# Kernel tuning notes

Measured on AMD Instinct MI355X. Metric: run time of the kernel, lower is better.

Reference implementation:

```python
import jax, jax.numpy as jnp
import numpy as np

EPS = 1e-5

def adain_norm(x):
    # per-(batch,channel) instance normalization over spatial dims (AdaIN projection)
    mean = jnp.mean(x, axis=(2, 3), keepdims=True)
    var = jnp.var(x, axis=(2, 3), keepdims=True)
    return (x - mean) / jnp.sqrt(var + EPS)

def conv1x1(x, w, b):
    # x: [B,C,H,W], w: [O,C], b: [O]
    return jnp.einsum('bchw,oc->bohw', x, w) + b[None, :, None, None]

def setup_inputs() -> dict:
    key = jax.random.key(0)
    ks = jax.random.split(key, 10)
    B, C, H, W = 4, 512, 64, 64
    s = 1.0 / np.sqrt(C)
    return {
        'x': jax.random.normal(ks[0], (B, C, H, W), jnp.float32),
        'y': jax.random.normal(ks[1], (B, C, H, W), jnp.float32),
        'f_w': jax.random.normal(ks[2], (C, C), jnp.float32) * s,
        'f_b': jnp.zeros((C,), jnp.float32),
        'g_w': jax.random.normal(ks[3], (C, C), jnp.float32) * s,
        'g_b': jnp.zeros((C,), jnp.float32),
        'h_w': jax.random.normal(ks[4], (C, C), jnp.float32) * s,
        'h_b': jnp.zeros((C,), jnp.float32),
        'out_w': jax.random.normal(ks[5], (C, C), jnp.float32) * s,
        'out_b': jnp.zeros((C,), jnp.float32),
    }

def reference(x, y, f_w, f_b, g_w, g_b, h_w, h_b, out_w, out_b):
    B, C, H, W = x.shape
    HW = H * W
    xn = adain_norm(x)
    yn = adain_norm(y)
    # 1x1 conv projections, flattened over spatial dims
    f = conv1x1(xn, f_w, f_b).reshape(B, C, HW)   # [B,C,HWx]
    g = conv1x1(yn, g_w, g_b).reshape(B, C, HW)   # [B,C,HWy]
    energy = jnp.einsum('bci,bcj->bij', f, g)     # [B,HWx,HWy]
    correlation = jax.nn.softmax(energy, axis=-1)
    h = conv1x1(y, h_w, h_b).reshape(B, C, HW)    # [B,C,HWy]
    # residual = h @ correlation^T -> [B,C,HWx]
    residual = jnp.einsum('bcj,bij->bci', h, correlation).reshape(B, C, H, W)
    residual = conv1x1(residual, out_w, out_b)
    return x + residual
```

## Files before the change

kernel.cpp:

```cpp
#include <hip/hip_runtime.h>
#include <stdint.h>

#define HW 4096
#define NC 512
#define NB 4

typedef __attribute__((ext_vector_type(8))) _Float16 f16x8;
typedef __attribute__((ext_vector_type(4))) float f32x4;
typedef __attribute__((ext_vector_type(4))) unsigned short ush4;
typedef __attribute__((ext_vector_type(8))) unsigned short ush8;

typedef __attribute__((address_space(1))) const void* as1_cvp;
typedef __attribute__((address_space(3))) void* as3_vp;

__device__ __forceinline__ unsigned short f2h(float f) {
  union { _Float16 h; unsigned short u; } c;
  c.h = (_Float16)f;
  return c.u;
}
__device__ __forceinline__ float h2f(unsigned short u) {
  union { unsigned short u; _Float16 h; } c;
  c.u = u;
  return (float)c.h;
}

__global__ __launch_bounds__(256) void moments_k(const float* __restrict__ x,
                                                 const float* __restrict__ y,
                                                 float* __restrict__ stats) {
  int bid = blockIdx.x;
  int tens = bid >> 11;
  int row = bid & 2047;
  const float* src = (tens ? y : x) + (size_t)row * HW;
  float s = 0.f, s2 = 0.f;
  for (int j = threadIdx.x; j < HW / 4; j += 256) {
    float4 v = ((const float4*)src)[j];
    s += (v.x + v.y) + (v.z + v.w);
    s2 += (v.x * v.x + v.y * v.y) + (v.z * v.z + v.w * v.w);
  }
  #pragma unroll
  for (int o = 32; o; o >>= 1) { s += __shfl_down(s, o); s2 += __shfl_down(s2, o); }
  __shared__ float rs[8];
  int w = threadIdx.x >> 6;
  if ((threadIdx.x & 63) == 0) { rs[w] = s; rs[4 + w] = s2; }
  __syncthreads();
  if (threadIdx.x == 0) {
    float S = (rs[0] + rs[1]) + (rs[2] + rs[3]);
    float S2 = (rs[4] + rs[5]) + (rs[6] + rs[7]);
    float mean = S * (1.f / HW);
    float var = S2 * (1.f / HW) - mean * mean;
    stats[tens * 4096 + row] = mean;
    stats[tens * 4096 + 2048 + row] = rsqrtf(var + 1e-5f);
  }
}

__global__ __launch_bounds__(256) void transnorm_k(const float* __restrict__ x,
                                                   const float* __restrict__ y,
                                                   const float* __restrict__ stats,
                                                   unsigned short* __restrict__ xnT,
                                                   unsigned short* __restrict__ ynT,
                                                   unsigned short* __restrict__ yH) {
  __shared__ float tile[64][65];
  __shared__ float ms[64], rsd[64];
  int zi = blockIdx.z;
  int b = zi >> 1, mode = zi & 1;
  int i0 = blockIdx.x * 64, c0 = blockIdx.y * 64;
  const float* src = mode ? y : x;
  int t = threadIdx.x;
  int c = t >> 2;
  int isub = (t & 3) << 4;
  if (t < 64) {
    int srow = (mode ? 4096 : 0) + b * NC + c0 + t;
    ms[t] = stats[srow];
    rsd[t] = stats[srow + 2048];
  }
  const float4* sp = (const float4*)(src + ((size_t)(b * NC + c0 + c)) * HW + i0 + isub);
  #pragma unroll
  for (int k = 0; k < 4; ++k) {
    float4 v = sp[k];
    int ib = isub + k * 4;
    tile[ib + 0][c] = v.x;
    tile[ib + 1][c] = v.y;
    tile[ib + 2][c] = v.z;
    tile[ib + 3][c] = v.w;
    if (mode) {
      ush4 yo;
      yo[0] = f2h(v.x); yo[1] = f2h(v.y); yo[2] = f2h(v.z); yo[3] = f2h(v.w);
      *(ush4*)(yH + ((size_t)(b * NC + c0 + c)) * HW + i0 + isub + k * 4) = yo;
    }
  }
  __syncthreads();
  int i = t >> 2;
  int cc = (t & 3) << 4;
  size_t obase = ((size_t)b * HW + i0 + i) * NC + c0 + cc;
  unsigned short* dst = mode ? ynT : xnT;
  #pragma unroll
  for (int h = 0; h < 2; ++h) {
    ush8 o;
    #pragma unroll
    for (int e = 0; e < 8; ++e) {
      int ce = cc + h * 8 + e;
      o[e] = f2h((tile[i][ce] - ms[ce]) * rsd[ce]);
    }
    *(ush8*)(dst + obase + h * 8) = o;
  }
}

__global__ __launch_bounds__(256) void castw_k(const float* __restrict__ fw,
                                               const float* __restrict__ gw,
                                               const float* __restrict__ hw_,
                                               const float* __restrict__ ow,
                                               unsigned short* __restrict__ fwT,
                                               unsigned short* __restrict__ gwT,
                                               unsigned short* __restrict__ hwT,
                                               unsigned short* __restrict__ owB) {
  __shared__ float tile[64][65];
  int which = blockIdx.z;
  const float* src = which == 0 ? fw : which == 1 ? gw : which == 2 ? hw_ : ow;
  unsigned short* dst = which == 0 ? fwT : which == 1 ? gwT : which == 2 ? hwT : owB;
  int r0 = blockIdx.x * 64, c0 = blockIdx.y * 64;
  int t = threadIdx.x;
  int r = t >> 2;
  int csub = (t & 3) << 4;
  const float4* sp = (const float4*)(src + (size_t)(r0 + r) * 512 + c0 + csub);
  if (which == 3) {
    #pragma unroll
    for (int k = 0; k < 4; ++k) {
      float4 v = sp[k];
      ush4 o;
      o[0] = f2h(v.x); o[1] = f2h(v.y); o[2] = f2h(v.z); o[3] = f2h(v.w);
      *(ush4*)(dst + (size_t)(r0 + r) * 512 + c0 + csub + k * 4) = o;
    }
    return;
  }
  #pragma unroll
  for (int k = 0; k < 4; ++k) {
    float4 v = sp[k];
    int cb = csub + k * 4;
    tile[cb + 0][r] = v.x;
    tile[cb + 1][r] = v.y;
    tile[cb + 2][r] = v.z;
    tile[cb + 3][r] = v.w;
  }
  __syncthreads();
  int cw = t >> 2;
  int rsub = (t & 3) << 4;
  #pragma unroll
  for (int h = 0; h < 2; ++h) {
    ush8 o;
    #pragma unroll
    for (int e = 0; e < 8; ++e) o[e] = f2h(tile[cw][rsub + h * 8 + e]);
    *(ush8*)(dst + (size_t)(c0 + cw) * 512 + r0 + rsub + h * 8) = o;
  }
}

__global__ __launch_bounds__(256) void repl_k(const unsigned short* __restrict__ W2,
                                              unsigned short* __restrict__ W2x2) {
  int idx = blockIdx.x * 256 + threadIdx.x;
  int o = idx >> 7;
  int k = (idx & 127) * 8;
  ush8 v = *(const ush8*)(W2 + (size_t)o * 512 + (k & 511));
  *(ush8*)(W2x2 + (size_t)o * 1024 + k) = v;
}

__global__ __launch_bounds__(256) void dotrows_h(const unsigned short* __restrict__ A,
                                                 const float* __restrict__ vec,
                                                 float* __restrict__ out) {
  int row = blockIdx.x * 4 + (threadIdx.x >> 6);
  int lane = threadIdx.x & 63;
  ush8 a = *(const ush8*)(A + (size_t)row * 512 + lane * 8);
  float s = 0.f;
  #pragma unroll
  for (int e = 0; e < 8; ++e) s += h2f(a[e]) * vec[lane * 8 + e];
  #pragma unroll
  for (int o = 32; o; o >>= 1) s += __shfl_down(s, o);
  if (lane == 0) out[row] = s;
}

__global__ __launch_bounds__(256) void b2_k(const float* __restrict__ Wf,
                                            const float* __restrict__ hb,
                                            const float* __restrict__ ob,
                                            float* __restrict__ out) {
  int row = blockIdx.x * 4 + (threadIdx.x >> 6);
  int lane = threadIdx.x & 63;
  const float4* a = (const float4*)(Wf + (size_t)row * 512) + lane * 2;
  float4 x0 = a[0], x1 = a[1];
  const float4* hv = (const float4*)hb + lane * 2;
  float4 h0 = hv[0], h1 = hv[1];
  float s = x0.x * h0.x + x0.y * h0.y + x0.z * h0.z + x0.w * h0.w
          + x1.x * h1.x + x1.y * h1.y + x1.z * h1.z + x1.w * h1.w;
  #pragma unroll
  for (int o = 32; o; o >>= 1) s += __shfl_down(s, o);
  if (lane == 0) out[row] = ob[row] + s;
}

__global__ __launch_bounds__(256) void softmax_h(unsigned short* __restrict__ S) {
  unsigned short* row = S + (size_t)blockIdx.x * HW;
  int t = threadIdx.x;
  ush8 a0 = *(const ush8*)(row + t * 16);
  ush8 a1 = *(const ush8*)(row + t * 16 + 8);
  float v[16];
  #pragma unroll
  for (int e = 0; e < 8; ++e) { v[e] = h2f(a0[e]); v[8 + e] = h2f(a1[e]); }
  float mx = -3.0e38f;
  #pragma unroll
  for (int e = 0; e < 16; ++e) mx = fmaxf(mx, v[e]);
  #pragma unroll
  for (int o = 32; o; o >>= 1) mx = fmaxf(mx, __shfl_down(mx, o));
  __shared__ float red[8];
  int w = t >> 6;
  if ((t & 63) == 0) red[w] = mx;
  __syncthreads();
  mx = fmaxf(fmaxf(red[0], red[1]), fmaxf(red[2], red[3]));
  float sum = 0.f;
  #pragma unroll
  for (int e = 0; e < 16; ++e) { v[e] = __expf(v[e] - mx); sum += v[e]; }
  #pragma unroll
  for (int o = 32; o; o >>= 1) sum += __shfl_down(sum, o);
  if ((t & 63) == 0) red[4 + w] = sum;
  __syncthreads();
  float inv = 1.f / ((red[4] + red[5]) + (red[6] + red[7]));
  ush8 o0, o1;
  #pragma unroll
  for (int e = 0; e < 8; ++e) { o0[e] = f2h(v[e] * inv); o1[e] = f2h(v[8 + e] * inv); }
  *(ush8*)(row + t * 16) = o0;
  *(ush8*)(row + t * 16 + 8) = o1;
}

__global__ __launch_bounds__(256, 2) void gemm_ntp(
    const unsigned short* __restrict__ A, long long sA, int lda,
    const unsigned short* __restrict__ Bm, long long sB, int ldb,
    void* __restrict__ Cp, long long sC, long long sCs, int ldc,
    int K, int out_f32, int ls,
    const float* __restrict__ bias_m, const float* __restrict__ bias_n,
    const float* __restrict__ add_src, long long sAdd,
    const unsigned short* __restrict__ B2, const float* __restrict__ bias_n2,
    int zsw) {
  __shared__ short lsA[2][128 * 64];
  __shared__ short lsB[2][128 * 64];
  const int t = threadIdx.x;
  const int lane = t & 63;
  const int w = t >> 6;
  const int wm = w >> 1, wn = w & 1;
  const long long bz = blockIdx.z;
  if ((int)bz >= zsw) { Bm = B2; bias_n = bias_n2; }
  const long long bg = bz >> ls;
  const int sp = (int)(bz - (bg << ls));
  const long long koff = (long long)sp * K;
  const unsigned short* Ab = A + bz * sA * (ls ? 0 : 1) + (ls ? bg * sA : 0) + koff
                           + (size_t)blockIdx.x * 128 * lda;
  const unsigned short* Bb = Bm + bg * sB + koff + (size_t)blockIdx.y * 128 * ldb;

  f32x4 zero = {0.f, 0.f, 0.f, 0.f};
  f32x4 acc[4][4];
  #pragma unroll
  for (int i = 0; i < 4; ++i)
    #pragma unroll
    for (int j = 0; j < 4; ++j) acc[i][j] = zero;

  const int nkt = K >> 6;

  auto STAGE = [&](int buf, int kt) {
    const int kbase = kt << 6;
    #pragma unroll
    for (int i = 0; i < 4; ++i) {
      int q = t + i * 256;
      int r = q >> 3, xx = q & 7;
      int gk = kbase + ((xx ^ (r & 7)) << 3);
      __builtin_amdgcn_global_load_lds((as1_cvp)(const void*)(Ab + (size_t)r * lda + gk),
                                       (as3_vp)(void*)(&lsA[buf][q << 3]), 16, 0, 0);
      __builtin_amdgcn_global_load_lds((as1_cvp)(const void*)(Bb + (size_t)r * ldb + gk),
                                       (as3_vp)(void*)(&lsB[buf][q << 3]), 16, 0, 0);
    }
  };

  STAGE(0, 0);
  __syncthreads();
  int cur = 0;
  for (int kt = 0; kt < nkt; ++kt) {
    if (kt + 1 < nkt) STAGE(cur ^ 1, kt + 1);
    #pragma unroll
    for (int ks = 0; ks < 2; ++ks) {
      f16x8 av[4], bv[4];
      const int xl = ks * 4 + (lane >> 4);
      const int rr = lane & 15;
      #pragma unroll
      for (int mb = 0; mb < 4; ++mb) {
        int row = wm * 64 + mb * 16 + rr;
        av[mb] = *(const f16x8*)&lsA[cur][(row << 6) + ((xl ^ (row & 7)) << 3)];
      }
      #pragma unroll
      for (int nb = 0; nb < 4; ++nb) {
        int row = wn * 64 + nb * 16 + rr;
        bv[nb] = *(const f16x8*)&lsB[cur][(row << 6) + ((xl ^ (row & 7)) << 3)];
      }
      __builtin_amdgcn_s_setprio(1);
      #pragma unroll
      for (int mb = 0; mb < 4; ++mb)
        #pragma unroll
        for (int nb = 0; nb < 4; ++nb)
          acc[mb][nb] = __builtin_amdgcn_mfma_f32_16x16x32_f16(av[mb], bv[nb], acc[mb][nb], 0, 0, 0);
      __builtin_amdgcn_s_setprio(0);
    }
    __syncthreads();
    cur ^= 1;
  }

  const int mb0 = blockIdx.x * 128 + wm * 64;
  const int nb0 = blockIdx.y * 128 + wn * 64;
  const int cn = lane & 15;
  const int rq = (lane >> 4) << 2;
  float* cf = (float*)Cp;
  unsigned short* ch = (unsigned short*)Cp;
  #pragma unroll
  for (int mb = 0; mb < 4; ++mb) {
    #pragma unroll
    for (int nb = 0; nb < 4; ++nb) {
      int n = nb0 + nb * 16 + cn;
      float bn = bias_n ? bias_n[n] : 0.f;
      #pragma unroll
      for (int r = 0; r < 4; ++r) {
        int m = mb0 + mb * 16 + rq + r;
        float vv = acc[mb][nb][r] + bn;
        if (bias_m) vv += bias_m[m];
        if (add_src) vv += add_src[bg * sAdd + (size_t)m * ldc + n];
        size_t off = (size_t)(bg * sC) + (size_t)sp * sCs + (size_t)m * ldc + n;
        if (out_f32) cf[off] = vv;
        else ch[off] = f2h(vv);
      }
    }
  }
}

__global__ __launch_bounds__(512, 1) void gemm_ntr(
    const unsigned short* __restrict__ A, long long sA, int lda,
    const unsigned short* __restrict__ Bm, long long sB, int ldb,
    void* __restrict__ Cp, long long sC, long long sCs, int ldc,
    int K, int out_f32, int ls,
    const float* __restrict__ bias_m,
    const float* __restrict__ bias_n, long long sBn,
    const float* __restrict__ add_src, long long sAdd) {
  __shared__ short lsA[3][256 * 64];
  __shared__ short lsB[3][128 * 64];
  const int t = threadIdx.x;
  const int lane = t & 63;
  const int w = t >> 6;
  const int wm = w >> 1, wn = w & 1;
  const long long bz = blockIdx.z;
  const long long bg = bz >> ls;
  const int sp = (int)(bz - (bg << ls));
  const long long koff = (long long)sp * K;
  const unsigned short* Ab = A + bg * sA + koff + (size_t)blockIdx.x * 256 * lda;
  const unsigned short* Bb = Bm + bg * sB + koff + (size_t)blockIdx.y * 128 * ldb;

  f32x4 zero = {0.f, 0.f, 0.f, 0.f};
  f32x4 acc[4][4];
  #pragma unroll
  for (int i = 0; i < 4; ++i)
    #pragma unroll
    for (int j = 0; j < 4; ++j) acc[i][j] = zero;

  const int nkt = K >> 6;

  auto STAGE = [&](int kt) {
    const int slot = kt % 3;
    const int kbase = kt << 6;
    #pragma unroll
    for (int i = 0; i < 4; ++i) {
      int q = t + i * 512;
      int r = q >> 3, xx = q & 7;
      int gk = kbase + ((xx ^ (r & 7)) << 3);
      __builtin_amdgcn_global_load_lds((as1_cvp)(const void*)(Ab + (size_t)r * lda + gk),
                                       (as3_vp)(void*)(&lsA[slot][q << 3]), 16, 0, 0);
    }
    #pragma unroll
    for (int i = 0; i < 2; ++i) {
      int q = t + i * 512;
      int r = q >> 3, xx = q & 7;
      int gk = kbase + ((xx ^ (r & 7)) << 3);
      __builtin_amdgcn_global_load_lds((as1_cvp)(const void*)(Bb + (size_t)r * ldb + gk),
                                       (as3_vp)(void*)(&lsB[slot][q << 3]), 16, 0, 0);
    }
  };

  auto COMPUTE = [&](int kt) {
    const int slot = kt % 3;
    #pragma unroll
    for (int ks = 0; ks < 2; ++ks) {
      f16x8 av[4], bv[4];
      const int xl = ks * 4 + (lane >> 4);
      const int rr = lane & 15;
      #pragma unroll
      for (int mb = 0; mb < 4; ++mb) {
        int row = wm * 64 + mb * 16 + rr;
        av[mb] = *(const f16x8*)&lsA[slot][(row << 6) + ((xl ^ (row & 7)) << 3)];
      }
      #pragma unroll
      for (int nb = 0; nb < 4; ++nb) {
        int row = wn * 64 + nb * 16 + rr;
        bv[nb] = *(const f16x8*)&lsB[slot][(row << 6) + ((xl ^ (row & 7)) << 3)];
      }
      __builtin_amdgcn_s_setprio(1);
      #pragma unroll
      for (int mb = 0; mb < 4; ++mb)
        #pragma unroll
        for (int nb = 0; nb < 4; ++nb)
          acc[mb][nb] = __builtin_amdgcn_mfma_f32_16x16x32_f16(av[mb], bv[nb], acc[mb][nb], 0, 0, 0);
      __builtin_amdgcn_s_setprio(0);
    }
  };

  STAGE(0);
  if (nkt > 1) {
    STAGE(1);
    asm volatile("s_waitcnt vmcnt(6)" ::: "memory");
  } else {
    asm volatile("s_waitcnt vmcnt(0)" ::: "memory");
  }
  __builtin_amdgcn_s_barrier();

  for (int kt = 0; kt < nkt; ++kt) {
    if (kt + 2 < nkt) STAGE(kt + 2);
    COMPUTE(kt);
    if (kt + 1 < nkt) {
      if (kt + 2 < nkt) asm volatile("s_waitcnt vmcnt(6)" ::: "memory");
      else              asm volatile("s_waitcnt vmcnt(0)" ::: "memory");
      __builtin_amdgcn_s_barrier();
    }
  }

  const int mb0 = blockIdx.x * 256 + wm * 64;
  const int nb0 = blockIdx.y * 128 + wn * 64;
  const int cn = lane & 15;
  const int rq = (lane >> 4) << 2;
  float* cf = (float*)Cp;
  unsigned short* ch = (unsigned short*)Cp;
  #pragma unroll
  for (int mb = 0; mb < 4; ++mb) {
    #pragma unroll
    for (int nb = 0; nb < 4; ++nb) {
      int n = nb0 + nb * 16 + cn;
      float bn = bias_n ? bias_n[bg * sBn + n] : 0.f;
      #pragma unroll
      for (int r = 0; r < 4; ++r) {
        int m = mb0 + mb * 16 + rq + r;
        float vv = acc[mb][nb][r] + bn;
        if (bias_m) vv += bias_m[m];
        if (add_src) vv += add_src[bg * sAdd + (size_t)m * ldc + n];
        size_t off = (size_t)(bg * sC) + (size_t)sp * sCs + (size_t)m * ldc + n;
        if (out_f32) cf[off] = vv;
        else ch[off] = f2h(vv);
      }
    }
  }
}

extern "C" void kernel_launch(void* const* d_in, const int* in_sizes, int n_in,
                              void* d_out, int out_size, void* d_ws, size_t ws_size,
                              hipStream_t stream) {
  const float* x = (const float*)d_in[0];
  const float* y = (const float*)d_in[1];
  const float* f_w = (const float*)d_in[2];
  const float* f_b = (const float*)d_in[3];
  const float* g_w = (const float*)d_in[4];
  const float* g_b = (const float*)d_in[5];
  const float* h_w = (const float*)d_in[6];
  const float* h_b = (const float*)d_in[7];
  const float* out_w = (const float*)d_in[8];
  const float* out_b = (const float*)d_in[9];
  float* out = (float*)d_out;
  (void)g_b;

  char* ws = (char*)d_ws;
  size_t off = 0;
  auto alloc = [&](size_t bytes) -> char* {
    char* p = ws + off;
    off += (bytes + 255) & ~(size_t)255;
    return p;
  };
  const size_t TN = (size_t)NB * HW * NC;
  const size_t WN = (size_t)512 * 512;
  float* stats = (float*)alloc(8192 * sizeof(float));
  unsigned short* fwT = (unsigned short*)alloc(WN * 2);
  unsigned short* gwT = (unsigned short*)alloc(WN * 2);
  unsigned short* hwT = (unsigned short*)alloc(WN * 2);
  unsigned short* owB = (unsigned short*)alloc(WN * 2);
  unsigned short* W1T = (unsigned short*)alloc(WN * 2);
  unsigned short* W2 = (unsigned short*)alloc(WN * 2);
  unsigned short* W2x2 = (unsigned short*)alloc((size_t)512 * 1024 * 2);
  float* vv = (float*)alloc(512 * 4);
  float* b2 = (float*)alloc(512 * 4);
  float* wj = (float*)alloc((size_t)NB * HW * 4);
  unsigned short* xnT = (unsigned short*)alloc(TN * 2);
  unsigned short* ynT = (unsigned short*)alloc(TN * 2);
  unsigned short* yH = (unsigned short*)alloc(TN * 2);
  unsigned short* fB = (unsigned short*)alloc(TN * 2);
  unsigned short* Zp = (unsigned short*)alloc((size_t)NB * HW * 1024 * 2);
  size_t remain = ws_size > off ? ws_size - off : 0;
  const size_t SB = (size_t)HW * HW * 2;
  int G, R = HW;
  if (remain >= 4 * SB)      { G = 4; }
  else if (remain >= 2 * SB) { G = 2; }
  else if (remain >= SB)     { G = 1; }
  else {
    G = 1;
    while (R > 128 && (size_t)R * HW * 2 > remain) R >>= 1;
  }
  unsigned short* Sh = (unsigned short*)alloc((size_t)G * R * HW * 2);
  if (off > ws_size) return;

  const long long PS = (long long)HW * NC;
  const int BIG = 1 << 30;

  castw_k<<<dim3(8, 8, 4), dim3(256), 0, stream>>>(f_w, g_w, h_w, out_w,
                                                   fwT, gwT, hwT, owB);
  moments_k<<<dim3(4096), dim3(256), 0, stream>>>(x, y, stats);
  transnorm_k<<<dim3(64, 8, 8), dim3(256), 0, stream>>>(x, y, stats, xnT, ynT, yH);

  dotrows_h<<<dim3(128), dim3(256), 0, stream>>>(gwT, f_b, vv);
  b2_k<<<dim3(128), dim3(256), 0, stream>>>(out_w, h_b, out_b, b2);
  gemm_ntp<<<dim3(4, 4, 1), dim3(256), 0, stream>>>(
      gwT, 0, 512, fwT, 0, 512, W1T, 0, 0, 512, 512, 0, 0,
      nullptr, nullptr, nullptr, 0, nullptr, nullptr, BIG);
  gemm_ntp<<<dim3(4, 4, 1), dim3(256), 0, stream>>>(
      owB, 0, 512, hwT, 0, 512, W2, 0, 0, 512, 512, 0, 0,
      nullptr, nullptr, nullptr, 0, nullptr, nullptr, BIG);
  repl_k<<<dim3(256), dim3(256), 0, stream>>>(W2, W2x2);
  dotrows_h<<<dim3(NB * HW / 4), dim3(256), 0, stream>>>(ynT, vv, wj);
  gemm_ntr<<<dim3(16, 4, NB), dim3(512), 0, stream>>>(
      xnT, PS, NC, W1T, 0, NC, fB, PS, 0, NC, NC, 0, 0,
      nullptr, nullptr, 0, nullptr, 0);

  for (int b0 = 0; b0 < NB; b0 += G) {
    for (int r0 = 0; r0 < HW; r0 += R) {
      if (R >= 256) {
        gemm_ntr<<<dim3(R / 256, HW / 128, G), dim3(512), 0, stream>>>(
            fB + ((size_t)b0 * HW + r0) * NC, PS, NC,
            ynT + (size_t)b0 * PS, PS, NC,
            Sh, (long long)R * HW, 0, HW, NC, 0, 0,
            nullptr, wj + (size_t)b0 * HW, HW, nullptr, 0);
        softmax_h<<<dim3(G * R), dim3(256), 0, stream>>>(Sh);
        gemm_ntr<<<dim3(R / 256, NC / 128, G * 2), dim3(512), 0, stream>>>(
            Sh, (long long)R * HW, HW,
            yH + (size_t)b0 * NC * HW, (long long)NC * HW, HW,
            Zp + ((size_t)b0 * HW + r0) * 1024, (long long)R * 1024, 512, 1024,
            HW / 2, 0, 1,
            nullptr, nullptr, 0, nullptr, 0);
      } else {
        gemm_ntp<<<dim3(R / 128, 32, G), dim3(256), 0, stream>>>(
            fB + ((size_t)b0 * HW + r0) * NC, PS, NC,
            ynT + (size_t)b0 * PS, PS, NC,
            Sh, (long long)R * HW, 0, HW, NC, 0, 0,
            nullptr, wj + (size_t)b0 * HW, nullptr, 0, nullptr, nullptr, BIG);
        softmax_h<<<dim3(G * R), dim3(256), 0, stream>>>(Sh);
        gemm_ntp<<<dim3(R / 128, 4, G * 2), dim3(256), 0, stream>>>(
            Sh, (long long)R * HW, HW,
            yH + (size_t)b0 * NC * HW, (long long)NC * HW, HW,
            Zp + ((size_t)b0 * HW + r0) * 1024, (long long)R * 1024, 512, 1024,
            HW / 2, 0, 1,
            nullptr, nullptr, nullptr, 0, nullptr, nullptr, BIG);
      }
    }
  }
  gemm_ntr<<<dim3(2, 32, NB), dim3(512), 0, stream>>>(
      W2x2, 0, 1024, Zp, (long long)HW * 1024, 1024,
      out, (long long)NC * HW, 0, HW, 1024, 1, 0,
      b2, nullptr, 0, x, (long long)NC * HW);
}
```

Baseline: 446.6 us.

## Enlarge GEMM tile to 256x256 with ping-pong interleaved load/MFMA schedule

Replaces the 256x128 triple-buffered GEMM kernel with a 256x256 tile, where each of 8 waves computes a 128x64 sub-tile. A/B tiles are double-buffered in halves, and the global-to-LDS loads are interleaved across four sub-phases of MFMA work with explicit barriers and waitcnts. The aim is higher arithmetic intensity per LDS byte and better overlap of memory with compute. In exchange it uses more accumulator registers and barriers, and launches half as many blocks in the N dimension, which may lower occupancy or grid fill. The loop assumes an even number of K tiles.

```diff
diff --git a/kernel.cpp b/kernel.cpp
--- a/kernel.cpp
+++ b/kernel.cpp
@@ -331,7 +331,7 @@
   }
 }
 
-__global__ __launch_bounds__(512, 1) void gemm_ntr(
+__global__ __launch_bounds__(512, 1) void gemm_nt8(
     const unsigned short* __restrict__ A, long long sA, int lda,
     const unsigned short* __restrict__ Bm, long long sB, int ldb,
     void* __restrict__ Cp, long long sC, long long sCs, int ldc,
@@ -339,103 +339,142 @@
     const float* __restrict__ bias_m,
     const float* __restrict__ bias_n, long long sBn,
     const float* __restrict__ add_src, long long sAdd) {
-  __shared__ short lsA[3][256 * 64];
-  __shared__ short lsB[3][128 * 64];
+  __shared__ short lsA[2][2][128 * 64];
+  __shared__ short lsB[2][2][128 * 64];
   const int t = threadIdx.x;
   const int lane = t & 63;
   const int w = t >> 6;
-  const int wm = w >> 1, wn = w & 1;
+  const int wm = w >> 2, wn = w & 3;
   const long long bz = blockIdx.z;
   const long long bg = bz >> ls;
   const int sp = (int)(bz - (bg << ls));
   const long long koff = (long long)sp * K;
   const unsigned short* Ab = A + bg * sA + koff + (size_t)blockIdx.x * 256 * lda;
-  const unsigned short* Bb = Bm + bg * sB + koff + (size_t)blockIdx.y * 128 * ldb;
+  const unsigned short* Bb = Bm + bg * sB + koff + (size_t)blockIdx.y * 256 * ldb;
 
   f32x4 zero = {0.f, 0.f, 0.f, 0.f};
-  f32x4 acc[4][4];
-  #pragma unroll
-  for (int i = 0; i < 4; ++i)
+  f32x4 acc[8][4];
+  #pragma unroll
+  for (int i = 0; i < 8; ++i)
     #pragma unroll
     for (int j = 0; j < 4; ++j) acc[i][j] = zero;
 
+  const int rr = lane & 15;
+  const int xl = lane >> 4;
   const int nkt = K >> 6;
 
-  auto STAGE = [&](int kt) {
-    const int slot = kt % 3;
-    const int kbase = kt << 6;
-    #pragma unroll
-    for (int i = 0; i < 4; ++i) {
-      int q = t + i * 512;
+  auto STAGE_A = [&](int kt, int hh) {
+    const int slot = kt & 1, kbase = kt << 6;
+    #pragma unroll
+    for (int i2 = 0; i2 < 2; ++i2) {
+      int q = t + i2 * 512;
       int r = q >> 3, xx = q & 7;
       int gk = kbase + ((xx ^ (r & 7)) << 3);
-      __builtin_amdgcn_global_load_lds((as1_cvp)(const void*)(Ab + (size_t)r * lda + gk),
-                                       (as3_vp)(void*)(&lsA[slot][q << 3]), 16, 0, 0);
-    }
-    #pragma unroll
-    for (int i = 0; i < 2; ++i) {
-      int q = t + i * 512;
+      __builtin_amdgcn_global_load_lds(
+          (as1_cvp)(const void*)(Ab + (size_t)(hh * 128 + r) * lda + gk),
+          (as3_vp)(void*)(&lsA[slot][hh][q << 3]), 16, 0, 0);
+    }
+  };
+  auto STAGE_B = [&](int kt, int hh) {
+    const int slot = kt & 1, kbase = kt << 6;
+    #pragma unroll
+    for (int i2 = 0; i2 < 2; ++i2) {
+      int q = t + i2 * 512;
       int r = q >> 3, xx = q & 7;
       int gk = kbase + ((xx ^ (r & 7)) << 3);
-      __builtin_amdgcn_global_load_lds((as1_cvp)(const void*)(Bb + (size_t)r * ldb + gk),
-                                       (as3_vp)(void*)(&lsB[slot][q << 3]), 16, 0, 0);
+      __builtin_amdgcn_global_load_lds(
+          (as1_cvp)(const void*)(Bb + (size_t)(hh * 128 + r) * ldb + gk),
+          (as3_vp)(void*)(&lsB[slot][hh][q << 3]), 16, 0, 0);
     }
   };
 
-  auto COMPUTE = [&](int kt) {
-    const int slot = kt % 3;
-    #pragma unroll
-    for (int ks = 0; ks < 2; ++ks) {
-      f16x8 av[4], bv[4];
-      const int xl = ks * 4 + (lane >> 4);
-      const int rr = lane & 15;
-      #pragma unroll
-      for (int mb = 0; mb < 4; ++mb) {
-        int row = wm * 64 + mb * 16 + rr;
-        av[mb] = *(const f16x8*)&lsA[slot][(row << 6) + ((xl ^ (row & 7)) << 3)];
+  f16x8 bv[4][2];
+  f16x8 av[2][2];
+  auto READ_B = [&](int slot) {
+    #pragma unroll
+    for (int nb = 0; nb < 4; ++nb)
+      #pragma unroll
+      for (int ks = 0; ks < 2; ++ks) {
+        int lr = (wn & 1) * 64 + nb * 16 + rr;
+        int cb = ks * 4 + xl;
+        bv[nb][ks] = *(const f16x8*)&lsB[slot][wn >> 1][(lr << 6) + ((cb ^ (lr & 7)) << 3)];
       }
-      #pragma unroll
-      for (int nb = 0; nb < 4; ++nb) {
-        int row = wn * 64 + nb * 16 + rr;
-        bv[nb] = *(const f16x8*)&lsB[slot][(row << 6) + ((xl ^ (row & 7)) << 3)];
+  };
+  auto READ_A = [&](int slot, int p) {
+    #pragma unroll
+    for (int j = 0; j < 2; ++j)
+      #pragma unroll
+      for (int ks = 0; ks < 2; ++ks) {
+        int lr = (2 * p + j) * 16 + rr;
+        int cb = ks * 4 + xl;
+        av[j][ks] = *(const f16x8*)&lsA[slot][wm][(lr << 6) + ((cb ^ (lr & 7)) << 3)];
       }
-      __builtin_amdgcn_s_setprio(1);
-      #pragma unroll
-      for (int mb = 0; mb < 4; ++mb)
+  };
+  auto MFMA16 = [&](int p) {
+    __builtin_amdgcn_s_setprio(1);
+    #pragma unroll
+    for (int j = 0; j < 2; ++j)
+      #pragma unroll
+      for (int nb = 0; nb < 4; ++nb)
         #pragma unroll
-        for (int nb = 0; nb < 4; ++nb)
-          acc[mb][nb] = __builtin_amdgcn_mfma_f32_16x16x32_f16(av[mb], bv[nb], acc[mb][nb], 0, 0, 0);
-      __builtin_amdgcn_s_setprio(0);
-    }
+        for (int ks = 0; ks < 2; ++ks)
+          acc[2 * p + j][nb] = __builtin_amdgcn_mfma_f32_16x16x32_f16(
+              av[j][ks], bv[nb][ks], acc[2 * p + j][nb], 0, 0, 0);
+    __builtin_amdgcn_s_setprio(0);
   };
 
-  STAGE(0);
+  STAGE_A(0, 0); STAGE_A(0, 1); STAGE_B(0, 0); STAGE_B(0, 1);
   if (nkt > 1) {
-    STAGE(1);
-    asm volatile("s_waitcnt vmcnt(6)" ::: "memory");
+    STAGE_B(1, 0); STAGE_B(1, 1);
+    asm volatile("s_waitcnt vmcnt(4)" ::: "memory");
   } else {
     asm volatile("s_waitcnt vmcnt(0)" ::: "memory");
   }
   __builtin_amdgcn_s_barrier();
 
-  for (int kt = 0; kt < nkt; ++kt) {
-    if (kt + 2 < nkt) STAGE(kt + 2);
-    COMPUTE(kt);
-    if (kt + 1 < nkt) {
-      if (kt + 2 < nkt) asm volatile("s_waitcnt vmcnt(6)" ::: "memory");
-      else              asm volatile("s_waitcnt vmcnt(0)" ::: "memory");
+  const int niter = nkt >> 1;
+  for (int it = 0; it < niter; ++it) {
+    const int t0 = 2 * it, t1 = 2 * it + 1;
+    #pragma unroll
+    for (int p = 0; p < 4; ++p) {
+      if (p == 0) READ_B(0);
+      READ_A(0, p);
+      if (p == 0)      { STAGE_A(t1, 0); STAGE_A(t1, 1); }
+      else if (p == 1) { if (t0 + 2 < nkt) STAGE_B(t0 + 2, 0); }
+      else if (p == 2) { if (t0 + 2 < nkt) STAGE_B(t0 + 2, 1); }
       __builtin_amdgcn_s_barrier();
-    }
-  }
-
-  const int mb0 = blockIdx.x * 256 + wm * 64;
-  const int nb0 = blockIdx.y * 128 + wn * 64;
+      asm volatile("s_waitcnt lgkmcnt(0)" ::: "memory");
+      __builtin_amdgcn_sched_barrier(0);
+      MFMA16(p);
+      if (p == 3) asm volatile("s_waitcnt vmcnt(4)" ::: "memory");
+      __builtin_amdgcn_s_barrier();
+    }
+    #pragma unroll
+    for (int p = 0; p < 4; ++p) {
+      if (p == 0) READ_B(1);
+      READ_A(1, p);
+      if (p == 0)      { if (t0 + 2 < nkt) STAGE_A(t0 + 2, 0); }
+      else if (p == 1) { if (t0 + 2 < nkt) STAGE_A(t0 + 2, 1); }
+      else if (p == 2) { if (t1 + 2 < nkt) STAGE_B(t1 + 2, 0); }
+      else             { if (t1 + 2 < nkt) STAGE_B(t1 + 2, 1); }
+      __builtin_amdgcn_s_barrier();
+      asm volatile("s_waitcnt lgkmcnt(0)" ::: "memory");
+      __builtin_amdgcn_sched_barrier(0);
+      MFMA16(p);
+      if (p == 3) asm volatile("s_waitcnt vmcnt(4)" ::: "memory");
+      __builtin_amdgcn_s_barrier();
+    }
+  }
+  asm volatile("s_waitcnt vmcnt(0)" ::: "memory");
+
+  const int mb0 = blockIdx.x * 256 + wm * 128;
+  const int nb0 = blockIdx.y * 256 + wn * 64;
   const int cn = lane & 15;
   const int rq = (lane >> 4) << 2;
   float* cf = (float*)Cp;
   unsigned short* ch = (unsigned short*)Cp;
   #pragma unroll
-  for (int mb = 0; mb < 4; ++mb) {
+  for (int mb = 0; mb < 8; ++mb) {
     #pragma unroll
     for (int nb = 0; nb < 4; ++nb) {
       int n = nb0 + nb * 16 + cn;
@@ -526,20 +565,20 @@
       nullptr, nullptr, nullptr, 0, nullptr, nullptr, BIG);
   repl_k<<<dim3(256), dim3(256), 0, stream>>>(W2, W2x2);
   dotrows_h<<<dim3(NB * HW / 4), dim3(256), 0, stream>>>(ynT, vv, wj);
-  gemm_ntr<<<dim3(16, 4, NB), dim3(512), 0, stream>>>(
+  gemm_nt8<<<dim3(16, 2, NB), dim3(512), 0, stream>>>(
       xnT, PS, NC, W1T, 0, NC, fB, PS, 0, NC, NC, 0, 0,
       nullptr, nullptr, 0, nullptr, 0);
 
   for (int b0 = 0; b0 < NB; b0 += G) {
     for (int r0 = 0; r0 < HW; r0 += R) {
       if (R >= 256) {
-        gemm_ntr<<<dim3(R / 256, HW / 128, G), dim3(512), 0, stream>>>(
+        gemm_nt8<<<dim3(R / 256, HW / 256, G), dim3(512), 0, stream>>>(
             fB + ((size_t)b0 * HW + r0) * NC, PS, NC,
             ynT + (size_t)b0 * PS, PS, NC,
             Sh, (long long)R * HW, 0, HW, NC, 0, 0,
             nullptr, wj + (size_t)b0 * HW, HW, nullptr, 0);
         softmax_h<<<dim3(G * R), dim3(256), 0, stream>>>(Sh);
-        gemm_ntr<<<dim3(R / 256, NC / 128, G * 2), dim3(512), 0, stream>>>(
+        gemm_nt8<<<dim3(R / 256, NC / 256, G * 2), dim3(512), 0, stream>>>(
             Sh, (long long)R * HW, HW,
             yH + (size_t)b0 * NC * HW, (long long)NC * HW, HW,
             Zp + ((size_t)b0 * HW + r0) * 1024, (long long)R * 1024, 512, 1024,
@@ -561,7 +600,7 @@
       }
     }
   }
-  gemm_ntr<<<dim3(2, 32, NB), dim3(512), 0, stream>>>(
+  gemm_nt8<<<dim3(2, 16, NB), dim3(512), 0, stream>>>(
       W2x2, 0, 1024, Zp, (long long)HW * 1024, 1024,
       out, (long long)NC * HW, 0, HW, 1024, 1, 0,
       b2, nullptr, 0, x, (long long)NC * HW);
```

New measurement: 455.0 us. Within noise of the previous version (+1.9%).
